# Kernel optimization log

Measured on AMD Instinct MI355X. Metric: run time of the kernel, lower is better.

## Reference

```python
import jax, jax.numpy as jnp
import numpy as np

B, T, D_IN = 16, 4096, 512
D_EMB, K = 256, 1024


def setup_inputs() -> dict:
    key = jax.random.key(0)
    k1, k2, k3, k4 = jax.random.split(key, 4)
    z_e = jax.random.normal(k1, (B, T, D_IN), dtype=jnp.float32)
    # nn.Embedding default init: N(0,1)
    codebook = jax.random.normal(k2, (K, D_EMB), dtype=jnp.float32)
    # nn.Linear(bias=False) weights, [out, in]
    W_down = jax.random.normal(k3, (D_EMB, D_IN), dtype=jnp.float32) / np.sqrt(D_IN)
    W_up = jax.random.normal(k4, (D_IN, D_EMB), dtype=jnp.float32) / np.sqrt(D_EMB)
    return {"z_e": z_e, "codebook": codebook, "W_down": W_down, "W_up": W_up}


def reference(z_e, codebook, W_down, W_up):
    # proj down: [B,T,D_IN] -> [B,T,D_EMB]
    z_e_down = jnp.einsum('btd,ed->bte', z_e, W_down)
    zf = z_e_down.reshape(-1, z_e_down.shape[-1])  # [BT, D_EMB]
    # squared L2 distances: ||z||^2 - 2 z.C^T + ||c||^2
    dist = (jnp.sum(zf * zf, axis=1, keepdims=True)
            - 2.0 * zf @ codebook.T
            + jnp.sum(codebook * codebook, axis=1)[None, :])  # [BT, K]
    code = jnp.argmin(dist, axis=1).reshape(z_e.shape[0], z_e.shape[1])  # [B, T]
    z_q_down = jnp.take(codebook, code, axis=0)  # [B, T, D_EMB]
    # training (freeze=False) path: VQ losses + straight-through estimator
    sq = (z_q_down - z_e_down) ** 2
    commitment_loss = jnp.mean(sq, axis=(1, 2))  # [B] (grad to z_e_down in torch)
    codebook_loss = jnp.mean(sq, axis=(1, 2))    # [B] (grad to codebook in torch)
    z_q_down_ste = z_e_down + jax.lax.stop_gradient(z_q_down - z_e_down)
    z_q = jnp.einsum('bte,de->btd', z_q_down_ste, W_up)  # [B, T, D_IN]
    return z_q, z_e_down, code, commitment_loss, codebook_loss
```

## Files before the change

kernel.cpp:

```cpp
#include <hip/hip_runtime.h>
#include <math.h>

#define BT_TOTAL 65536
#define DIN 512
#define DEMB 256
#define KCODES 1024

typedef __attribute__((ext_vector_type(8))) short short8;
typedef __attribute__((ext_vector_type(4))) float floatx4;

__device__ __forceinline__ unsigned short f2bf(float x) {
    unsigned u = __float_as_uint(x);
    unsigned r = u + 0x7fffu + ((u >> 16) & 1u);
    return (unsigned short)(r >> 16);
}
__device__ __forceinline__ float bf2f(unsigned short h) {
    return __uint_as_float(((unsigned)h) << 16);
}

__global__ __launch_bounds__(256) void cnorm_kernel(const float* __restrict__ cbook,
                                                    float* __restrict__ cnorm,
                                                    float* __restrict__ out_loss) {
    const int k = blockIdx.x;
    const int tid = threadIdx.x;
    float v = cbook[k * DEMB + tid];
    v *= v;
#pragma unroll
    for (int o = 32; o > 0; o >>= 1) v += __shfl_down(v, o);
    __shared__ float ps[4];
    if ((tid & 63) == 0) ps[tid >> 6] = v;
    __syncthreads();
    if (tid == 0) cnorm[k] = ps[0] + ps[1] + ps[2] + ps[3];
    if (k == 0 && tid < 32) out_loss[tid] = 0.0f;
}

__global__ __launch_bounds__(256) void swz_kernel(const float* __restrict__ Bt,
                                                  unsigned short* __restrict__ hi,
                                                  unsigned short* __restrict__ lo,
                                                  int K, int total) {
    const int o = blockIdx.x * 256 + threadIdx.x;
    if (o >= total) return;
    const int j = o & 7;
    const int l = (o >> 3) & 63;
    const int r = o >> 9;
    const int kst = K >> 5;
    const int s = r % kst;
    const int t = r / kst;
    const int c = t * 16 + (l & 15);
    const int k = s * 32 + (l >> 4) * 8 + j;
    const float v = Bt[(size_t)c * K + k];
    const unsigned short h = f2bf(v);
    hi[o] = (unsigned short)h;
    lo[o] = f2bf(v - bf2f(h));
}

template <int KD, int NSTR>
__global__ __launch_bounds__(256) void gemm_rowdot(const float* __restrict__ A,
                                                   const float* __restrict__ Bt,
                                                   float* __restrict__ C) {
    __shared__ __align__(16) float As[64][36];
    __shared__ __align__(16) float Bs[64][36];
    const int tid = threadIdx.x;
    const int tx = tid & 15, ty = tid >> 4;
    const int rowBase = blockIdx.x * 64;
    const int colBase = blockIdx.y * 64;
    const int lr = tid >> 2;
    const int lk = (tid & 3) * 8;
    float acc[4][4] = {};
    for (int k0 = 0; k0 < KD; k0 += 32) {
        const float4 a0 = *(const float4*)(A + (size_t)(rowBase + lr) * KD + k0 + lk);
        const float4 a1 = *(const float4*)(A + (size_t)(rowBase + lr) * KD + k0 + lk + 4);
        const float4 b0 = *(const float4*)(Bt + (size_t)(colBase + lr) * KD + k0 + lk);
        const float4 b1 = *(const float4*)(Bt + (size_t)(colBase + lr) * KD + k0 + lk + 4);
        __syncthreads();
        *(float4*)&As[lr][lk] = a0;
        *(float4*)&As[lr][lk + 4] = a1;
        *(float4*)&Bs[lr][lk] = b0;
        *(float4*)&Bs[lr][lk + 4] = b1;
        __syncthreads();
#pragma unroll
        for (int e = 0; e < 32; e += 4) {
            float4 va[4], vb[4];
#pragma unroll
            for (int i = 0; i < 4; ++i) va[i] = *(const float4*)&As[4 * ty + i][e];
#pragma unroll
            for (int j = 0; j < 4; ++j) vb[j] = *(const float4*)&Bs[4 * tx + j][e];
#pragma unroll
            for (int i = 0; i < 4; ++i)
#pragma unroll
                for (int j = 0; j < 4; ++j) {
                    acc[i][j] = fmaf(va[i].x, vb[j].x, acc[i][j]);
                    acc[i][j] = fmaf(va[i].y, vb[j].y, acc[i][j]);
                    acc[i][j] = fmaf(va[i].z, vb[j].z, acc[i][j]);
                    acc[i][j] = fmaf(va[i].w, vb[j].w, acc[i][j]);
                }
        }
    }
#pragma unroll
    for (int i = 0; i < 4; ++i) {
        float4 o = make_float4(acc[i][0], acc[i][1], acc[i][2], acc[i][3]);
        *(float4*)(C + (size_t)(rowBase + 4 * ty + i) * NSTR + colBase + 4 * tx) = o;
    }
}

__global__ __launch_bounds__(256) void gemm_down_mfma(const float* __restrict__ A,
                                                      const unsigned short* __restrict__ bhi,
                                                      const unsigned short* __restrict__ blo,
                                                      float* __restrict__ C) {
    __shared__ __align__(16) short lds_h[16][512];
    __shared__ __align__(16) short lds_l[16][512];
    const int tid = threadIdx.x;
    const int lane = tid & 63, wv = tid >> 6;
    const int m = lane & 15, q = lane >> 4;
    const int rowBase = blockIdx.x * 64 + wv * 16;

    floatx4 acc[16];
#pragma unroll
    for (int t = 0; t < 16; ++t) acc[t] = (floatx4){0.f, 0.f, 0.f, 0.f};

    for (int s = 0; s < 16; ++s) {
        const float4* ap = (const float4*)(A + (size_t)(rowBase + m) * DIN + s * 32 + q * 8);
        const float4 v0 = ap[0], v1 = ap[1];
        __syncthreads();
#pragma unroll
        for (int i = 0; i < 8; ++i) {
            const int c = wv * 8 + i;
            const int t = c >> 1;
            const unsigned short* src = (c & 1) ? blo : bhi;
            const short8 vst = *(const short8*)(src + ((size_t)(t * 16 + s) * 64 + lane) * 8);
            short* dst = (c & 1) ? &lds_l[t][lane * 8] : &lds_h[t][lane * 8];
            *(short8*)dst = vst;
        }
        const float xs[8] = {v0.x, v0.y, v0.z, v0.w, v1.x, v1.y, v1.z, v1.w};
        short8 ahi, alo;
#pragma unroll
        for (int j = 0; j < 8; ++j) {
            const unsigned short h = f2bf(xs[j]);
            ahi[j] = (short)h;
            alo[j] = (short)f2bf(xs[j] - bf2f(h));
        }
        __syncthreads();
#pragma unroll
        for (int t = 0; t < 16; ++t) {
            const short8 bh = *(const short8*)&lds_h[t][lane * 8];
            const short8 bl = *(const short8*)&lds_l[t][lane * 8];
            acc[t] = __builtin_amdgcn_mfma_f32_16x16x32_bf16(ahi, bh, acc[t], 0, 0, 0);
            acc[t] = __builtin_amdgcn_mfma_f32_16x16x32_bf16(alo, bh, acc[t], 0, 0, 0);
            acc[t] = __builtin_amdgcn_mfma_f32_16x16x32_bf16(ahi, bl, acc[t], 0, 0, 0);
        }
    }
#pragma unroll
    for (int t = 0; t < 16; ++t)
#pragma unroll
        for (int r = 0; r < 4; ++r)
            C[(size_t)(rowBase + q * 4 + r) * DEMB + t * 16 + m] = acc[t][r];
}

__global__ __launch_bounds__(256) void dist_mfma(const float* __restrict__ zed,
                                                 const unsigned short* __restrict__ chi,
                                                 const unsigned short* __restrict__ clo,
                                                 const float* __restrict__ cnorm,
                                                 float* __restrict__ out_code,
                                                 float* __restrict__ out_loss) {
    __shared__ __align__(16) short lds_h[2][8][512];
    __shared__ __align__(16) short lds_l[2][8][512];
    __shared__ float cn_s[KCODES];
    __shared__ float znorm_s[64];
    __shared__ float blockSum;
    const int tid = threadIdx.x;
    const int lane = tid & 63, wv = tid >> 6;
    const int m = lane & 15, q = lane >> 4;
    const int rowBase = blockIdx.x * 64 + wv * 16;

    *(float4*)&cn_s[tid * 4] = *(const float4*)(cnorm + tid * 4);
    if (tid == 0) blockSum = 0.f;

    short8 ahi[8], alo[8];
    float zn = 0.f;
#pragma unroll
    for (int s = 0; s < 8; ++s) {
        const float4* ap = (const float4*)(zed + (size_t)(rowBase + m) * DEMB + s * 32 + q * 8);
        const float4 v0 = ap[0], v1 = ap[1];
        const float xs[8] = {v0.x, v0.y, v0.z, v0.w, v1.x, v1.y, v1.z, v1.w};
#pragma unroll
        for (int j = 0; j < 8; ++j) {
            const unsigned short h = f2bf(xs[j]);
            ahi[s][j] = (short)h;
            alo[s][j] = (short)f2bf(xs[j] - bf2f(h));
            zn = fmaf(xs[j], xs[j], zn);
        }
    }
    zn += __shfl_xor(zn, 16, 64);
    zn += __shfl_xor(zn, 32, 64);
    if (q == 0) znorm_s[wv * 16 + m] = zn;

#pragma unroll
    for (int i = 0; i < 4; ++i) {
        const int c = wv * 4 + i;
        const int s = c >> 1;
        const unsigned short* src = (c & 1) ? clo : chi;
        const short8 vst = *(const short8*)(src + ((size_t)(0 * 8 + s) * 64 + lane) * 8);
        short* dst = (c & 1) ? &lds_l[0][s][lane * 8] : &lds_h[0][s][lane * 8];
        *(short8*)dst = vst;
    }
    __syncthreads();

    float bestv[4] = {INFINITY, INFINITY, INFINITY, INFINITY};
    int besti[4] = {0, 0, 0, 0};
    int buf = 0;

    for (int t = 0; t < 64; ++t) {
        if (t < 63) {
#pragma unroll
            for (int i = 0; i < 4; ++i) {
                const int c = wv * 4 + i;
                const int s = c >> 1;
                const unsigned short* src = (c & 1) ? clo : chi;
                const short8 vst =
                    *(const short8*)(src + ((size_t)((t + 1) * 8 + s) * 64 + lane) * 8);
                short* dst = (c & 1) ? &lds_l[buf ^ 1][s][lane * 8]
                                     : &lds_h[buf ^ 1][s][lane * 8];
                *(short8*)dst = vst;
            }
        }
        floatx4 acc0 = (floatx4){0.f, 0.f, 0.f, 0.f};
        floatx4 acc1 = (floatx4){0.f, 0.f, 0.f, 0.f};
#pragma unroll
        for (int s = 0; s < 8; s += 2) {
            const short8 bh0 = *(const short8*)&lds_h[buf][s][lane * 8];
            const short8 bl0 = *(const short8*)&lds_l[buf][s][lane * 8];
            const short8 bh1 = *(const short8*)&lds_h[buf][s + 1][lane * 8];
            const short8 bl1 = *(const short8*)&lds_l[buf][s + 1][lane * 8];
            acc0 = __builtin_amdgcn_mfma_f32_16x16x32_bf16(ahi[s], bh0, acc0, 0, 0, 0);
            acc0 = __builtin_amdgcn_mfma_f32_16x16x32_bf16(alo[s], bh0, acc0, 0, 0, 0);
            acc0 = __builtin_amdgcn_mfma_f32_16x16x32_bf16(ahi[s], bl0, acc0, 0, 0, 0);
            acc1 = __builtin_amdgcn_mfma_f32_16x16x32_bf16(ahi[s + 1], bh1, acc1, 0, 0, 0);
            acc1 = __builtin_amdgcn_mfma_f32_16x16x32_bf16(alo[s + 1], bh1, acc1, 0, 0, 0);
            acc1 = __builtin_amdgcn_mfma_f32_16x16x32_bf16(ahi[s + 1], bl1, acc1, 0, 0, 0);
        }
        const int code = t * 16 + m;
        const float cn = cn_s[code];
#pragma unroll
        for (int r = 0; r < 4; ++r) {
            const float d = fmaf(-2.f, acc0[r] + acc1[r], cn);
            if (d < bestv[r]) { bestv[r] = d; besti[r] = code; }
        }
        __syncthreads();
        buf ^= 1;
    }

#pragma unroll
    for (int off = 1; off < 16; off <<= 1) {
#pragma unroll
        for (int r = 0; r < 4; ++r) {
            const float ov = __shfl_xor(bestv[r], off, 16);
            const int oi = __shfl_xor(besti[r], off, 16);
            if (ov < bestv[r] || (ov == bestv[r] && oi < besti[r])) {
                bestv[r] = ov;
                besti[r] = oi;
            }
        }
    }
    if (m == 0) {
        float ls = 0.f;
#pragma unroll
        for (int r = 0; r < 4; ++r) {
            const int lrow = q * 4 + r;
            out_code[rowBase + lrow] = (float)besti[r];
            ls += bestv[r] + znorm_s[wv * 16 + lrow];
        }
        atomicAdd(&blockSum, ls);
    }
    __syncthreads();
    if (tid == 0) {
        const int b = blockIdx.x >> 6;
        const float v = blockSum * (1.0f / (4096.0f * 256.0f));
        atomicAdd(&out_loss[b], v);
        atomicAdd(&out_loss[16 + b], v);
    }
}

__global__ __launch_bounds__(256) void gather_kernel(const float* __restrict__ P,
                                                     const float* __restrict__ code_f,
                                                     float* __restrict__ zq) {
    const int lane = threadIdx.x & 63;
    const int row = blockIdx.x * 4 + (threadIdx.x >> 6);
    const int c = (int)code_f[row];
    const float4* src = (const float4*)(P + (size_t)c * DIN);
    float4* dst = (float4*)(zq + (size_t)row * DIN);
    dst[lane] = src[lane];
    dst[lane + 64] = src[lane + 64];
}

extern "C" void kernel_launch(void* const* d_in, const int* in_sizes, int n_in,
                              void* d_out, int out_size, void* d_ws, size_t ws_size,
                              hipStream_t stream) {
    const float* z_e = (const float*)d_in[0];
    const float* cbook = (const float*)d_in[1];
    const float* W_down = (const float*)d_in[2];
    const float* W_up = (const float*)d_in[3];

    float* out = (float*)d_out;
    float* out_zq = out;
    float* out_zed = out + 33554432;
    float* out_code = out_zed + 16777216;
    float* out_loss = out_code + 65536;

    char* wsb = (char*)d_ws;
    float* cnorm = (float*)wsb;
    unsigned short* cb_hi = (unsigned short*)(wsb + 4096);
    unsigned short* cb_lo = (unsigned short*)(wsb + 4096 + 524288);
    unsigned short* wd_hi = (unsigned short*)(wsb + 4096 + 2 * 524288);
    unsigned short* wd_lo = (unsigned short*)(wsb + 4096 + 2 * 524288 + 262144);
    float* P = (float*)(wsb + 4096);

    cnorm_kernel<<<KCODES, 256, 0, stream>>>(cbook, cnorm, out_loss);
    swz_kernel<<<1024, 256, 0, stream>>>(cbook, cb_hi, cb_lo, 256, 262144);
    swz_kernel<<<512, 256, 0, stream>>>(W_down, wd_hi, wd_lo, 512, 131072);

    gemm_down_mfma<<<BT_TOTAL / 64, 256, 0, stream>>>(z_e, wd_hi, wd_lo, out_zed);
    dist_mfma<<<BT_TOTAL / 64, 256, 0, stream>>>(out_zed, cb_hi, cb_lo, cnorm,
                                                 out_code, out_loss);
    gemm_rowdot<256, 512><<<dim3(16, 8), 256, 0, stream>>>(cbook, W_up, P);
    gather_kernel<<<BT_TOTAL / 4, 256, 0, stream>>>(P, out_code, out_zq);
}
```

Before: 510.4 us.

## Switch distance kernel to 32x32x16 MFMA with 128-row blocks

The distance kernel now uses 32x32x16 bf16 MFMA tiles, so each wave covers 32 rows and 32 codes. Blocks handle 128 rows, which halves the block count and doubles the reuse of each codebook tile staged in LDS. The codebook swizzle kernel gets a matching 32-wide layout. Global prefetch is moved into registers ahead of the MFMA work, with s_setprio raised around the MFMA section. The cost is more register pressure (16 A fragments, 16-wide accumulators, 16 best values) and occupancy capped by launch_bounds(256,2).

```diff
diff --git a/kernel.cpp b/kernel.cpp
--- a/kernel.cpp
+++ b/kernel.cpp
@@ -8,6 +8,7 @@
 
 typedef __attribute__((ext_vector_type(8))) short short8;
 typedef __attribute__((ext_vector_type(4))) float floatx4;
+typedef __attribute__((ext_vector_type(16))) float floatx16;
 
 __device__ __forceinline__ unsigned short f2bf(float x) {
     unsigned u = __float_as_uint(x);
@@ -54,6 +55,26 @@
     lo[o] = f2bf(v - bf2f(h));
 }
 
+__global__ __launch_bounds__(256) void swz32_kernel(const float* __restrict__ Bt,
+                                                    unsigned short* __restrict__ hi,
+                                                    unsigned short* __restrict__ lo,
+                                                    int K, int total) {
+    const int o = blockIdx.x * 256 + threadIdx.x;
+    if (o >= total) return;
+    const int j = o & 7;
+    const int l = (o >> 3) & 63;
+    const int r = o >> 9;
+    const int kst = K >> 4;
+    const int s = r % kst;
+    const int t = r / kst;
+    const int c = t * 32 + (l & 31);
+    const int k = s * 16 + (l >> 5) * 8 + j;
+    const float v = Bt[(size_t)c * K + k];
+    const unsigned short h = f2bf(v);
+    hi[o] = (unsigned short)h;
+    lo[o] = f2bf(v - bf2f(h));
+}
+
 template <int KD, int NSTR>
 __global__ __launch_bounds__(256) void gemm_rowdot(const float* __restrict__ A,
                                                    const float* __restrict__ Bt,
@@ -156,31 +177,48 @@
             C[(size_t)(rowBase + q * 4 + r) * DEMB + t * 16 + m] = acc[t][r];
 }
 
-__global__ __launch_bounds__(256) void dist_mfma(const float* __restrict__ zed,
-                                                 const unsigned short* __restrict__ chi,
-                                                 const unsigned short* __restrict__ clo,
-                                                 const float* __restrict__ cnorm,
-                                                 float* __restrict__ out_code,
-                                                 float* __restrict__ out_loss) {
+#define DIST_CHUNKS(BASE)                                                                     \
+    {                                                                                         \
+        _Pragma("unroll") for (int s8 = 0; s8 < 8; s8 += 2) {                                 \
+            const short8 bh0 = *(const short8*)&lds_h[buf][s8][lane * 8];                     \
+            const short8 bl0 = *(const short8*)&lds_l[buf][s8][lane * 8];                     \
+            const short8 bh1 = *(const short8*)&lds_h[buf][s8 + 1][lane * 8];                 \
+            const short8 bl1 = *(const short8*)&lds_l[buf][s8 + 1][lane * 8];                 \
+            accA = __builtin_amdgcn_mfma_f32_32x32x16_bf16(ahi[BASE + s8], bh0, accA, 0, 0, 0);     \
+            accB = __builtin_amdgcn_mfma_f32_32x32x16_bf16(ahi[BASE + s8 + 1], bh1, accB, 0, 0, 0); \
+            accA = __builtin_amdgcn_mfma_f32_32x32x16_bf16(alo[BASE + s8], bh0, accA, 0, 0, 0);     \
+            accB = __builtin_amdgcn_mfma_f32_32x32x16_bf16(alo[BASE + s8 + 1], bh1, accB, 0, 0, 0); \
+            accA = __builtin_amdgcn_mfma_f32_32x32x16_bf16(ahi[BASE + s8], bl0, accA, 0, 0, 0);     \
+            accB = __builtin_amdgcn_mfma_f32_32x32x16_bf16(ahi[BASE + s8 + 1], bl1, accB, 0, 0, 0); \
+        }                                                                                     \
+    }
+
+__global__ __launch_bounds__(256, 2) void dist_mfma(const float* __restrict__ zed,
+                                                    const unsigned short* __restrict__ chi,
+                                                    const unsigned short* __restrict__ clo,
+                                                    const float* __restrict__ cnorm,
+                                                    float* __restrict__ out_code,
+                                                    float* __restrict__ out_loss) {
     __shared__ __align__(16) short lds_h[2][8][512];
     __shared__ __align__(16) short lds_l[2][8][512];
     __shared__ float cn_s[KCODES];
-    __shared__ float znorm_s[64];
+    __shared__ float znorm_s[4][32];
     __shared__ float blockSum;
     const int tid = threadIdx.x;
     const int lane = tid & 63, wv = tid >> 6;
-    const int m = lane & 15, q = lane >> 4;
-    const int rowBase = blockIdx.x * 64 + wv * 16;
+    const int cc = lane & 31, half = lane >> 5;
+    const int rowBase = blockIdx.x * 128 + wv * 32;
 
     *(float4*)&cn_s[tid * 4] = *(const float4*)(cnorm + tid * 4);
     if (tid == 0) blockSum = 0.f;
 
-    short8 ahi[8], alo[8];
+    short8 ahi[16], alo[16];
     float zn = 0.f;
-#pragma unroll
-    for (int s = 0; s < 8; ++s) {
-        const float4* ap = (const float4*)(zed + (size_t)(rowBase + m) * DEMB + s * 32 + q * 8);
-        const float4 v0 = ap[0], v1 = ap[1];
+    const float* arow = zed + (size_t)(rowBase + cc) * DEMB + half * 8;
+#pragma unroll
+    for (int s = 0; s < 16; ++s) {
+        const float4 v0 = *(const float4*)(arow + s * 16);
+        const float4 v1 = *(const float4*)(arow + s * 16 + 4);
         const float xs[8] = {v0.x, v0.y, v0.z, v0.w, v1.x, v1.y, v1.z, v1.w};
 #pragma unroll
         for (int j = 0; j < 8; ++j) {
@@ -190,90 +228,106 @@
             zn = fmaf(xs[j], xs[j], zn);
         }
     }
-    zn += __shfl_xor(zn, 16, 64);
     zn += __shfl_xor(zn, 32, 64);
-    if (q == 0) znorm_s[wv * 16 + m] = zn;
+    if (half == 0) znorm_s[wv][cc] = zn;
 
 #pragma unroll
     for (int i = 0; i < 4; ++i) {
         const int c = wv * 4 + i;
-        const int s = c >> 1;
+        const int s8 = c >> 1;
         const unsigned short* src = (c & 1) ? clo : chi;
-        const short8 vst = *(const short8*)(src + ((size_t)(0 * 8 + s) * 64 + lane) * 8);
-        short* dst = (c & 1) ? &lds_l[0][s][lane * 8] : &lds_h[0][s][lane * 8];
+        const short8 vst = *(const short8*)(src + ((size_t)s8 * 64 + lane) * 8);
+        short* dst = (c & 1) ? &lds_l[0][s8][lane * 8] : &lds_h[0][s8][lane * 8];
         *(short8*)dst = vst;
     }
     __syncthreads();
 
-    float bestv[4] = {INFINITY, INFINITY, INFINITY, INFINITY};
-    int besti[4] = {0, 0, 0, 0};
+    floatx16 accA, accB;
+    float bestv[16];
+    int besti[16];
+#pragma unroll
+    for (int r = 0; r < 16; ++r) {
+        accA[r] = 0.f;
+        accB[r] = 0.f;
+        bestv[r] = INFINITY;
+        besti[r] = 0;
+    }
     int buf = 0;
 
-    for (int t = 0; t < 64; ++t) {
-        if (t < 63) {
+    for (int ph = 0; ph < 64; ++ph) {
+        const int t = ph >> 1;
+        short8 pf[4];
+        if (ph < 63) {
+            const int tn = (ph + 1) >> 1;
+            const int sb = ((ph + 1) & 1) * 8;
 #pragma unroll
             for (int i = 0; i < 4; ++i) {
                 const int c = wv * 4 + i;
-                const int s = c >> 1;
+                const int s8 = c >> 1;
                 const unsigned short* src = (c & 1) ? clo : chi;
-                const short8 vst =
-                    *(const short8*)(src + ((size_t)((t + 1) * 8 + s) * 64 + lane) * 8);
-                short* dst = (c & 1) ? &lds_l[buf ^ 1][s][lane * 8]
-                                     : &lds_h[buf ^ 1][s][lane * 8];
-                *(short8*)dst = vst;
+                pf[i] = *(const short8*)(src + ((size_t)(tn * 16 + sb + s8) * 64 + lane) * 8);
             }
         }
-        floatx4 acc0 = (floatx4){0.f, 0.f, 0.f, 0.f};
-        floatx4 acc1 = (floatx4){0.f, 0.f, 0.f, 0.f};
-#pragma unroll
-        for (int s = 0; s < 8; s += 2) {
-            const short8 bh0 = *(const short8*)&lds_h[buf][s][lane * 8];
-            const short8 bl0 = *(const short8*)&lds_l[buf][s][lane * 8];
-            const short8 bh1 = *(const short8*)&lds_h[buf][s + 1][lane * 8];
-            const short8 bl1 = *(const short8*)&lds_l[buf][s + 1][lane * 8];
-            acc0 = __builtin_amdgcn_mfma_f32_16x16x32_bf16(ahi[s], bh0, acc0, 0, 0, 0);
-            acc0 = __builtin_amdgcn_mfma_f32_16x16x32_bf16(alo[s], bh0, acc0, 0, 0, 0);
-            acc0 = __builtin_amdgcn_mfma_f32_16x16x32_bf16(ahi[s], bl0, acc0, 0, 0, 0);
-            acc1 = __builtin_amdgcn_mfma_f32_16x16x32_bf16(ahi[s + 1], bh1, acc1, 0, 0, 0);
-            acc1 = __builtin_amdgcn_mfma_f32_16x16x32_bf16(alo[s + 1], bh1, acc1, 0, 0, 0);
-            acc1 = __builtin_amdgcn_mfma_f32_16x16x32_bf16(ahi[s + 1], bl1, acc1, 0, 0, 0);
-        }
-        const int code = t * 16 + m;
-        const float cn = cn_s[code];
-#pragma unroll
-        for (int r = 0; r < 4; ++r) {
-            const float d = fmaf(-2.f, acc0[r] + acc1[r], cn);
-            if (d < bestv[r]) { bestv[r] = d; besti[r] = code; }
+        __builtin_amdgcn_s_setprio(1);
+        if ((ph & 1) == 0) {
+            DIST_CHUNKS(0)
+        } else {
+            DIST_CHUNKS(8)
+        }
+        __builtin_amdgcn_s_setprio(0);
+        if (ph & 1) {
+            const float cn = cn_s[t * 32 + cc];
+            const int code = t * 32 + cc;
+#pragma unroll
+            for (int r = 0; r < 16; ++r) {
+                const float d = fmaf(-2.f, accA[r] + accB[r], cn);
+                if (d < bestv[r]) {
+                    bestv[r] = d;
+                    besti[r] = code;
+                }
+                accA[r] = 0.f;
+                accB[r] = 0.f;
+            }
+        }
+        if (ph < 63) {
+#pragma unroll
+            for (int i = 0; i < 4; ++i) {
+                const int c = wv * 4 + i;
+                const int s8 = c >> 1;
+                short* dst = (c & 1) ? &lds_l[buf ^ 1][s8][lane * 8]
+                                     : &lds_h[buf ^ 1][s8][lane * 8];
+                *(short8*)dst = pf[i];
+            }
         }
         __syncthreads();
         buf ^= 1;
     }
 
 #pragma unroll
-    for (int off = 1; off < 16; off <<= 1) {
-#pragma unroll
-        for (int r = 0; r < 4; ++r) {
-            const float ov = __shfl_xor(bestv[r], off, 16);
-            const int oi = __shfl_xor(besti[r], off, 16);
+    for (int off = 1; off < 32; off <<= 1) {
+#pragma unroll
+        for (int r = 0; r < 16; ++r) {
+            const float ov = __shfl_xor(bestv[r], off, 64);
+            const int oi = __shfl_xor(besti[r], off, 64);
             if (ov < bestv[r] || (ov == bestv[r] && oi < besti[r])) {
                 bestv[r] = ov;
                 besti[r] = oi;
             }
         }
     }
-    if (m == 0) {
+    if (cc == 0) {
         float ls = 0.f;
 #pragma unroll
-        for (int r = 0; r < 4; ++r) {
-            const int lrow = q * 4 + r;
-            out_code[rowBase + lrow] = (float)besti[r];
-            ls += bestv[r] + znorm_s[wv * 16 + lrow];
+        for (int r = 0; r < 16; ++r) {
+            const int row = (r & 3) + 8 * (r >> 2) + 4 * half;
+            out_code[rowBase + row] = (float)besti[r];
+            ls += bestv[r] + znorm_s[wv][row];
         }
         atomicAdd(&blockSum, ls);
     }
     __syncthreads();
     if (tid == 0) {
-        const int b = blockIdx.x >> 6;
+        const int b = blockIdx.x >> 5;
         const float v = blockSum * (1.0f / (4096.0f * 256.0f));
         atomicAdd(&out_loss[b], v);
         atomicAdd(&out_loss[16 + b], v);
@@ -315,12 +369,12 @@
     float* P = (float*)(wsb + 4096);
 
     cnorm_kernel<<<KCODES, 256, 0, stream>>>(cbook, cnorm, out_loss);
-    swz_kernel<<<1024, 256, 0, stream>>>(cbook, cb_hi, cb_lo, 256, 262144);
+    swz32_kernel<<<1024, 256, 0, stream>>>(cbook, cb_hi, cb_lo, 256, 262144);
     swz_kernel<<<512, 256, 0, stream>>>(W_down, wd_hi, wd_lo, 512, 131072);
 
     gemm_down_mfma<<<BT_TOTAL / 64, 256, 0, stream>>>(z_e, wd_hi, wd_lo, out_zed);
-    dist_mfma<<<BT_TOTAL / 64, 256, 0, stream>>>(out_zed, cb_hi, cb_lo, cnorm,
-                                                 out_code, out_loss);
+    dist_mfma<<<BT_TOTAL / 128, 256, 0, stream>>>(out_zed, cb_hi, cb_lo, cnorm,
+                                                  out_code, out_loss);
     gemm_rowdot<256, 512><<<dim3(16, 8), 256, 0, stream>>>(cbook, W_up, P);
     gather_kernel<<<BT_TOTAL / 4, 256, 0, stream>>>(P, out_code, out_zq);
 }
```

Result: faster. 491.4 us (-3.7%).
